# Kernel optimization log

Measured on AMD Instinct MI355X. Metric: run time of the kernel, lower is better.

## Reference

```python
import jax, jax.numpy as jnp
import numpy as np

D, A, V, H, FFH = 512, 256, 256, 1, 256
B, S, VOCAB = 4096, 50, 100000


def _layer_norm(x, g, b, eps=1e-6):
    mu = jnp.mean(x, axis=-1, keepdims=True)
    var = jnp.mean((x - mu) ** 2, axis=-1, keepdims=True)
    return (x - mu) / jnp.sqrt(var + eps) * g + b


def setup_inputs() -> dict:
    key = jax.random.key(0)
    ks = jax.random.split(key, 12)
    s = 0.02
    return {
        "embed_table": jax.random.normal(ks[0], (VOCAB, D), jnp.float32),
        "idx": jax.random.randint(ks[1], (B, S), 0, VOCAB, dtype=jnp.int32),
        "lengths": jax.random.randint(ks[2], (B,), 0, S, dtype=jnp.int32),
        "W1": jax.random.normal(ks[3], (D, FFH), jnp.float32) * s,
        "b1": jnp.zeros((FFH,), jnp.float32),
        "W2": jax.random.normal(ks[4], (FFH, D), jnp.float32) * s,
        "b2": jnp.zeros((D,), jnp.float32),
        "ln1_g": jnp.ones((D,), jnp.float32),
        "ln1_b": jnp.zeros((D,), jnp.float32),
        "W_qkv": jax.random.normal(ks[5], (D, 2 * A + V), jnp.float32) * s,
        "b_qkv": jnp.zeros((2 * A + V,), jnp.float32),
        "W_o": jax.random.normal(ks[6], (V, D), jnp.float32) * s,
        "b_o": jnp.zeros((D,), jnp.float32),
        "ln2_g": jnp.ones((D,), jnp.float32),
        "ln2_b": jnp.zeros((D,), jnp.float32),
    }


def reference(embed_table, idx, lengths, W1, b1, W2, b2, ln1_g, ln1_b,
              W_qkv, b_qkv, W_o, b_o, ln2_g, ln2_b):
    # neighbor validity mask; guaranteed >= 1 valid neighbor per node
    mask = jnp.arange(S)[None, :] <= lengths[:, None]          # [B,S] bool

    # irregular gather of neighbor embeddings into padded tensor
    x = embed_table[idx]                                       # [B,S,D]

    # FeedForward (relu -> linear) + residual + LayerNorm
    ff = jnp.maximum(jnp.einsum('bsd,df->bsf', x, W1) + b1, 0.0)
    ff = jnp.einsum('bsf,fd->bsd', ff, W2) + b2
    ff = _layer_norm(ff + x, ln1_g, ln1_b)                     # [B,S,D]

    # MultiHeadSelfAttention (combined QKV projection)
    qkv = jnp.einsum('bsd,dc->bsc', ff, W_qkv) + b_qkv         # [B,S,2A+V]
    q, k, v = qkv[..., :A], qkv[..., A:2 * A], qkv[..., 2 * A:]
    q = q.reshape(B, S, H, A // H)
    k = k.reshape(B, S, H, A // H)
    v = v.reshape(B, S, H, V // H)
    scale = jnp.asarray(np.sqrt(D // H), q.dtype)              # AllenNLP scale
    scores = jnp.einsum('bqhd,bkhd->bhqk', q / scale, k)       # [B,H,S,S]
    scores = jnp.where(mask[:, None, None, :], scores, jnp.asarray(-1e9, scores.dtype))
    attn = jax.nn.softmax(scores, axis=-1)
    ctx = jnp.einsum('bhqk,bkhd->bqhd', attn, v).reshape(B, S, V)
    attn_out = jnp.einsum('bsv,vd->bsd', ctx, W_o) + b_o

    out = _layer_norm(attn_out + ff, ln2_g, ln2_b)             # [B,S,D]

    # masked mean pool over neighbors
    m = mask[..., None].astype(out.dtype)                      # [B,S,1]
    pooled = jnp.sum(out * m, axis=1) / jnp.maximum(jnp.sum(m, axis=1), 1e-13)
    return pooled                                              # [B,D]
```

## Files before the change

### kernel.cpp

```cpp
#include <hip/hip_runtime.h>

typedef __bf16 bf16x8 __attribute__((ext_vector_type(8)));
typedef float float4v __attribute__((ext_vector_type(4)));
typedef unsigned short ushort4v __attribute__((ext_vector_type(4)));
typedef unsigned short ushort8v __attribute__((ext_vector_type(8)));

#define K_D 512
#define K_S 50

__device__ __forceinline__ float b2f(unsigned short u) {
  union { unsigned int u32; float f; } v; v.u32 = ((unsigned int)u) << 16; return v.f;
}
__device__ __forceinline__ unsigned short f2b(float f) {
  __bf16 h = (__bf16)f;
  return __builtin_bit_cast(unsigned short, h);
}

__device__ __forceinline__ bf16x8 ldfrag(const unsigned short* buf, int E, int r0, int k0, int lane) {
  int row = r0 + (lane & 15);
  int kb = (k0 + ((lane >> 4) << 3)) << 1;
  return *(const bf16x8*)(buf + row * E + ((kb ^ ((row & 7) << 4)) >> 1));
}

__global__ void prep_weights(const float* __restrict__ src, unsigned short* __restrict__ dst,
                             int K, int N) {
  int KT = K >> 5;
  int total = (N >> 4) * KT * 64;
  int t = blockIdx.x * blockDim.x + threadIdx.x;
  if (t >= total) return;
  int l = t & 63;
  int kt = (t >> 6) % KT;
  int nt = (t >> 6) / KT;
  int kbase = kt * 32 + ((l >> 4) << 3);
  int col = nt * 16 + (l & 15);
  ushort8v o;
  #pragma unroll
  for (int j = 0; j < 8; ++j) o[j] = f2b(src[(size_t)(kbase + j) * N + col]);
  *(ushort8v*)(dst + (size_t)t * 8) = o;
}

template<int NT, int KS, int MT, int SLOTS, int APRE>
__device__ __forceinline__ void mmN(const unsigned short* Ab, int EA,
                                    const bf16x8* __restrict__ Wf, int wnb, int KT, int l,
                                    float4v* acc) {
  if constexpr (SLOTS == 2) {
    bf16x8 p0[NT], p1[NT];
    #pragma unroll
    for (int n = 0; n < NT; ++n) {
      p0[n] = Wf[(size_t)((wnb + n) * KT) * 64 + l];
      p1[n] = Wf[(size_t)((wnb + n) * KT + 1) * 64 + l];
    }
    bf16x8 a0[MT], a1[MT];
    if constexpr (APRE) {
      #pragma unroll
      for (int m = 0; m < MT; ++m) {
        a0[m] = ldfrag(Ab, EA, m * 16, 0, l);
        a1[m] = ldfrag(Ab, EA, m * 16, 32, l);
      }
    }
    #pragma unroll 1
    for (int kt = 0; kt < KS; kt += 2) {
      {
        if constexpr (!APRE) {
          #pragma unroll
          for (int m = 0; m < MT; ++m) a0[m] = ldfrag(Ab, EA, m * 16, kt * 32, l);
        }
        #pragma unroll
        for (int n = 0; n < NT; ++n) {
          #pragma unroll
          for (int m = 0; m < MT; ++m)
            acc[m * NT + n] = __builtin_amdgcn_mfma_f32_16x16x32_bf16(a0[m], p0[n], acc[m * NT + n], 0, 0, 0);
        }
        if (kt + 2 < KS) {
          #pragma unroll
          for (int n = 0; n < NT; ++n)
            p0[n] = Wf[(size_t)((wnb + n) * KT + kt + 2) * 64 + l];
          if constexpr (APRE) {
            #pragma unroll
            for (int m = 0; m < MT; ++m) a0[m] = ldfrag(Ab, EA, m * 16, (kt + 2) * 32, l);
          }
        }
      }
      {
        if constexpr (!APRE) {
          #pragma unroll
          for (int m = 0; m < MT; ++m) a1[m] = ldfrag(Ab, EA, m * 16, (kt + 1) * 32, l);
        }
        #pragma unroll
        for (int n = 0; n < NT; ++n) {
          #pragma unroll
          for (int m = 0; m < MT; ++m)
            acc[m * NT + n] = __builtin_amdgcn_mfma_f32_16x16x32_bf16(a1[m], p1[n], acc[m * NT + n], 0, 0, 0);
        }
        if (kt + 3 < KS) {
          #pragma unroll
          for (int n = 0; n < NT; ++n)
            p1[n] = Wf[(size_t)((wnb + n) * KT + kt + 3) * 64 + l];
          if constexpr (APRE) {
            #pragma unroll
            for (int m = 0; m < MT; ++m) a1[m] = ldfrag(Ab, EA, m * 16, (kt + 3) * 32, l);
          }
        }
      }
    }
  } else {
    bf16x8 bn[NT];
    #pragma unroll
    for (int n = 0; n < NT; ++n) bn[n] = Wf[(size_t)((wnb + n) * KT) * 64 + l];
    #pragma unroll 1
    for (int kt = 0; kt < KS; ++kt) {
      bf16x8 a[MT];
      #pragma unroll
      for (int m = 0; m < MT; ++m) a[m] = ldfrag(Ab, EA, m * 16, kt * 32, l);
      #pragma unroll
      for (int n = 0; n < NT; ++n) {
        #pragma unroll
        for (int m = 0; m < MT; ++m)
          acc[m * NT + n] = __builtin_amdgcn_mfma_f32_16x16x32_bf16(a[m], bn[n], acc[m * NT + n], 0, 0, 0);
      }
      if (kt + 1 < KS) {
        #pragma unroll
        for (int n = 0; n < NT; ++n)
          bn[n] = Wf[(size_t)((wnb + n) * KT + kt + 1) * 64 + l];
      }
    }
  }
}

__device__ __forceinline__ void ln_pass(unsigned short* sXbuf, const float* __restrict__ g,
                                        const float* __restrict__ bb, int w, int l, int nrows) {
  float gv[8], bv[8];
  {
    const float4* g4 = (const float4*)(g + l * 8);
    const float4* b4 = (const float4*)(bb + l * 8);
    float4 a0 = g4[0], a1 = g4[1], c0 = b4[0], c1 = b4[1];
    gv[0] = a0.x; gv[1] = a0.y; gv[2] = a0.z; gv[3] = a0.w;
    gv[4] = a1.x; gv[5] = a1.y; gv[6] = a1.z; gv[7] = a1.w;
    bv[0] = c0.x; bv[1] = c0.y; bv[2] = c0.z; bv[3] = c0.w;
    bv[4] = c1.x; bv[5] = c1.y; bv[6] = c1.z; bv[7] = c1.w;
  }
  #pragma unroll 1
  for (int r = w; r < nrows; r += 16) {
    int e = r * 512 + (((l << 4) ^ ((r & 7) << 4)) >> 1);
    ushort8v x = *(const ushort8v*)(sXbuf + e);
    float v[8];
    float s = 0.f, s2 = 0.f;
    #pragma unroll
    for (int j = 0; j < 8; ++j) { v[j] = b2f(x[j]); s += v[j]; s2 += v[j] * v[j]; }
    #pragma unroll
    for (int off = 1; off < 64; off <<= 1) { s += __shfl_xor(s, off); s2 += __shfl_xor(s2, off); }
    float mu = s * (1.f / 512.f);
    float var = s2 * (1.f / 512.f) - mu * mu;
    float rstd = rsqrtf(var + 1e-6f);
    ushort8v o;
    #pragma unroll
    for (int j = 0; j < 8; ++j) o[j] = f2b((v[j] - mu) * rstd * gv[j] + bv[j]);
    *(ushort8v*)(sXbuf + e) = o;
  }
}

template<int MT>
__device__ __forceinline__ void body(
    unsigned short* sX, unsigned short* sQ, unsigned short* sK,
    float* sS, unsigned short* sP,
    const float* __restrict__ embed, const int* __restrict__ gidx,
    const float* __restrict__ b1, const float* __restrict__ b2,
    const float* __restrict__ ln1g, const float* __restrict__ ln1b,
    const float* __restrict__ bqkv, const float* __restrict__ bo,
    const float* __restrict__ ln2g, const float* __restrict__ ln2b,
    const unsigned short* __restrict__ w1f, const unsigned short* __restrict__ w2f,
    const unsigned short* __restrict__ wqkvf, const unsigned short* __restrict__ wof,
    float* __restrict__ out, int tid, int w, int l, int b, int len) {

  constexpr int S2 = (MT <= 3) ? 2 : 1;
  constexpr int AP1 = (MT <= 3) ? 1 : 0;
  constexpr int AP2 = (MT <= 2) ? 1 : 0;

  {
    const int sub = tid >> 7;
    const int c0 = (tid & 127) << 2;
    #pragma unroll 2
    for (int it = 0; it < 2 * MT; ++it) {
      int r = it * 8 + sub;
      float4 v = make_float4(0.f, 0.f, 0.f, 0.f);
      if (r <= len) {
        int row = gidx[b * K_S + r];
        v = *(const float4*)(embed + (size_t)row * K_D + c0);
      }
      ushort4v o;
      o[0] = f2b(v.x); o[1] = f2b(v.y); o[2] = f2b(v.z); o[3] = f2b(v.w);
      *(ushort4v*)(sX + r * 512 + (((c0 << 1) ^ ((r & 7) << 4)) >> 1)) = o;
    }
  }
  __syncthreads();

  {
    float4v acc[MT];
    #pragma unroll
    for (int i = 0; i < MT; ++i) acc[i] = (float4v){0.f, 0.f, 0.f, 0.f};
    mmN<1, 16, MT, 2, AP1>(sX, 512, (const bf16x8*)w1f, w, 16, l, acc);
    int col = w * 16 + (l & 15);
    float bias = b1[col];
    #pragma unroll
    for (int m = 0; m < MT; ++m) {
      int r0 = m * 16 + ((l >> 4) << 2);
      #pragma unroll
      for (int j = 0; j < 4; ++j) {
        int r = r0 + j;
        float v = fmaxf(acc[m][j] + bias, 0.f);
        sQ[r * 256 + (((col << 1) ^ ((r & 7) << 4)) >> 1)] = f2b(v);
      }
    }
  }
  __syncthreads();

  {
    float4v acc[2 * MT];
    #pragma unroll
    for (int i = 0; i < 2 * MT; ++i) acc[i] = (float4v){0.f, 0.f, 0.f, 0.f};
    mmN<2, 8, MT, S2, AP2>(sQ, 256, (const bf16x8*)w2f, w * 2, 8, l, acc);
    #pragma unroll
    for (int n = 0; n < 2; ++n) {
      int col = (w * 2 + n) * 16 + (l & 15);
      float bias = b2[col];
      #pragma unroll
      for (int m = 0; m < MT; ++m) {
        int r0 = m * 16 + ((l >> 4) << 2);
        #pragma unroll
        for (int j = 0; j < 4; ++j) {
          int r = r0 + j;
          int e = r * 512 + (((col << 1) ^ ((r & 7) << 4)) >> 1);
          float v = acc[m * 2 + n][j] + bias + b2f(sX[e]);
          sX[e] = f2b(v);
        }
      }
    }
  }
  __syncthreads();
  ln_pass(sX, ln1g, ln1b, w, l, 16 * MT);
  __syncthreads();

  {
    const bf16x8* Wf = (const bf16x8*)wqkvf;
    float4v accQ[MT], accK[MT];
    #pragma unroll
    for (int i = 0; i < MT; ++i) {
      accQ[i] = (float4v){0.f, 0.f, 0.f, 0.f};
      accK[i] = (float4v){0.f, 0.f, 0.f, 0.f};
    }
    const size_t baseQ = (size_t)(w) * 16 * 64 + l;
    const size_t baseK = (size_t)(16 + w) * 16 * 64 + l;
    if constexpr (MT <= 2) {
      bf16x8 q0 = Wf[baseQ],       k0 = Wf[baseK];
      bf16x8 q1 = Wf[baseQ + 64],  k1 = Wf[baseK + 64];
      bf16x8 a0[MT], a1[MT];
      #pragma unroll
      for (int m = 0; m < MT; ++m) {
        a0[m] = ldfrag(sX, 512, m * 16, 0, l);
        a1[m] = ldfrag(sX, 512, m * 16, 32, l);
      }
      #pragma unroll 1
      for (int kt = 0; kt < 16; kt += 2) {
        {
          #pragma unroll
          for (int m = 0; m < MT; ++m) accQ[m] = __builtin_amdgcn_mfma_f32_16x16x32_bf16(a0[m], q0, accQ[m], 0, 0, 0);
          #pragma unroll
          for (int m = 0; m < MT; ++m) accK[m] = __builtin_amdgcn_mfma_f32_16x16x32_bf16(a0[m], k0, accK[m], 0, 0, 0);
          if (kt + 2 < 16) {
            q0 = Wf[baseQ + (size_t)(kt + 2) * 64];
            k0 = Wf[baseK + (size_t)(kt + 2) * 64];
            #pragma unroll
            for (int m = 0; m < MT; ++m) a0[m] = ldfrag(sX, 512, m * 16, (kt + 2) * 32, l);
          }
        }
        {
          #pragma unroll
          for (int m = 0; m < MT; ++m) accQ[m] = __builtin_amdgcn_mfma_f32_16x16x32_bf16(a1[m], q1, accQ[m], 0, 0, 0);
          #pragma unroll
          for (int m = 0; m < MT; ++m) accK[m] = __builtin_amdgcn_mfma_f32_16x16x32_bf16(a1[m], k1, accK[m], 0, 0, 0);
          if (kt + 3 < 16) {
            q1 = Wf[baseQ + (size_t)(kt + 3) * 64];
            k1 = Wf[baseK + (size_t)(kt + 3) * 64];
            #pragma unroll
            for (int m = 0; m < MT; ++m) a1[m] = ldfrag(sX, 512, m * 16, (kt + 3) * 32, l);
          }
        }
      }
    } else {
      bf16x8 q0 = Wf[baseQ], k0 = Wf[baseK];
      #pragma unroll 1
      for (int kt = 0; kt < 16; ++kt) {
        bf16x8 a[MT];
        #pragma unroll
        for (int m = 0; m < MT; ++m) a[m] = ldfrag(sX, 512, m * 16, kt * 32, l);
        #pragma unroll
        for (int m = 0; m < MT; ++m) accQ[m] = __builtin_amdgcn_mfma_f32_16x16x32_bf16(a[m], q0, accQ[m], 0, 0, 0);
        #pragma unroll
        for (int m = 0; m < MT; ++m) accK[m] = __builtin_amdgcn_mfma_f32_16x16x32_bf16(a[m], k0, accK[m], 0, 0, 0);
        if (kt + 1 < 16) {
          q0 = Wf[baseQ + (size_t)(kt + 1) * 64];
          k0 = Wf[baseK + (size_t)(kt + 1) * 64];
        }
      }
    }
    const float qscale = 0.044194173824159216f;
    int col = w * 16 + (l & 15);
    float biasQ = bqkv[col];
    float biasK = bqkv[256 + col];
    #pragma unroll
    for (int m = 0; m < MT; ++m) {
      int r0 = m * 16 + ((l >> 4) << 2);
      #pragma unroll
      for (int j = 0; j < 4; ++j) {
        int r = r0 + j;
        sQ[r * 256 + (((col << 1) ^ ((r & 7) << 4)) >> 1)] = f2b((accQ[m][j] + biasQ) * qscale);
        sK[r * 256 + (((col << 1) ^ ((r & 7) << 4)) >> 1)] = f2b(accK[m][j] + biasK);
      }
    }
  }
  __syncthreads();

  if ((w >> 2) < MT) {
    float4v acc = (float4v){0.f, 0.f, 0.f, 0.f};
    int n0 = (w & 3) * 16;
    int m0 = (w >> 2) * 16;
    bf16x8 b0 = ldfrag(sK, 256, n0, 0, l),  aq0 = ldfrag(sQ, 256, m0, 0, l);
    bf16x8 b1 = ldfrag(sK, 256, n0, 32, l), aq1 = ldfrag(sQ, 256, m0, 32, l);
    #pragma unroll 1
    for (int kt = 0; kt < 8; kt += 2) {
      acc = __builtin_amdgcn_mfma_f32_16x16x32_bf16(aq0, b0, acc, 0, 0, 0);
      if (kt + 2 < 8) {
        b0 = ldfrag(sK, 256, n0, (kt + 2) * 32, l);
        aq0 = ldfrag(sQ, 256, m0, (kt + 2) * 32, l);
      }
      acc = __builtin_amdgcn_mfma_f32_16x16x32_bf16(aq1, b1, acc, 0, 0, 0);
      if (kt + 3 < 8) {
        b1 = ldfrag(sK, 256, n0, (kt + 3) * 32, l);
        aq1 = ldfrag(sQ, 256, m0, (kt + 3) * 32, l);
      }
    }
    int col = n0 + (l & 15);
    int r0 = m0 + ((l >> 4) << 2);
    #pragma unroll
    for (int j = 0; j < 4; ++j) {
      int r = r0 + j;
      sS[r * 64 + (((col << 2) ^ ((r & 7) << 4)) >> 2)] = acc[j];
    }
  }
  float4v accV[MT];
  {
    #pragma unroll
    for (int i = 0; i < MT; ++i) accV[i] = (float4v){0.f, 0.f, 0.f, 0.f};
    mmN<1, 16, MT, 2, AP1>(sX, 512, (const bf16x8*)wqkvf, 32 + w, 16, l, accV);
  }
  __syncthreads();

  {
    const bool valid = (l <= len);
    #pragma unroll 1
    for (int r = w; r < 16 * MT; r += 16) {
      float s = valid ? sS[r * 64 + (((l << 2) ^ ((r & 7) << 4)) >> 2)] : -1e30f;
      float mx = s;
      #pragma unroll
      for (int off = 1; off < 64; off <<= 1) mx = fmaxf(mx, __shfl_xor(mx, off));
      float p = valid ? __expf(s - mx) : 0.f;
      float sum = p;
      #pragma unroll
      for (int off = 1; off < 64; off <<= 1) sum += __shfl_xor(sum, off);
      sP[r * 64 + (((l << 1) ^ ((r & 7) << 4)) >> 1)] = f2b(p / sum);
    }
    int c = w * 16 + (l & 15);
    float biasV = bqkv[512 + c];
    #pragma unroll
    for (int m = 0; m < MT; ++m) {
      int r0 = m * 16 + ((l >> 4) << 2);
      ushort4v o;
      #pragma unroll
      for (int j = 0; j < 4; ++j) o[j] = f2b(accV[m][j] + biasV);
      *(ushort4v*)(sK + c * 64 + (((r0 << 1) ^ ((c & 7) << 4)) >> 1)) = o;
    }
    #pragma unroll
    for (int m = MT; m < 4; ++m) {
      int r0 = m * 16 + ((l >> 4) << 2);
      ushort4v o; o[0] = 0; o[1] = 0; o[2] = 0; o[3] = 0;
      *(ushort4v*)(sK + c * 64 + (((r0 << 1) ^ ((c & 7) << 4)) >> 1)) = o;
    }
  }
  __syncthreads();

  {
    float4v acc[MT];
    #pragma unroll
    for (int i = 0; i < MT; ++i) acc[i] = (float4v){0.f, 0.f, 0.f, 0.f};
    #pragma unroll
    for (int kt = 0; kt < 2; ++kt) {
      bf16x8 bfr = ldfrag(sK, 64, w * 16, kt * 32, l);
      #pragma unroll
      for (int m = 0; m < MT; ++m) {
        bf16x8 a = ldfrag(sP, 64, m * 16, kt * 32, l);
        acc[m] = __builtin_amdgcn_mfma_f32_16x16x32_bf16(a, bfr, acc[m], 0, 0, 0);
      }
    }
    int col = w * 16 + (l & 15);
    #pragma unroll
    for (int m = 0; m < MT; ++m) {
      int r0 = m * 16 + ((l >> 4) << 2);
      #pragma unroll
      for (int j = 0; j < 4; ++j) {
        int r = r0 + j;
        sQ[r * 256 + (((col << 1) ^ ((r & 7) << 4)) >> 1)] = f2b(acc[m][j]);
      }
    }
  }
  __syncthreads();

  {
    float4v acc[2 * MT];
    #pragma unroll
    for (int i = 0; i < 2 * MT; ++i) acc[i] = (float4v){0.f, 0.f, 0.f, 0.f};
    mmN<2, 8, MT, S2, AP2>(sQ, 256, (const bf16x8*)wof, w * 2, 8, l, acc);
    #pragma unroll
    for (int n = 0; n < 2; ++n) {
      int col = (w * 2 + n) * 16 + (l & 15);
      float bias = bo[col];
      #pragma unroll
      for (int m = 0; m < MT; ++m) {
        int r0 = m * 16 + ((l >> 4) << 2);
        #pragma unroll
        for (int j = 0; j < 4; ++j) {
          int r = r0 + j;
          int e = r * 512 + (((col << 1) ^ ((r & 7) << 4)) >> 1);
          float v = acc[m * 2 + n][j] + bias + b2f(sX[e]);
          sX[e] = f2b(v);
        }
      }
    }
  }
  __syncthreads();
  ln_pass(sX, ln2g, ln2b, w, l, 16 * MT);
  __syncthreads();

  {
    int col = tid & 511;
    int half = tid >> 9;
    float sum = 0.f;
    for (int s = half; s <= len; s += 2)
      sum += b2f(sX[s * 512 + (((col << 1) ^ ((s & 7) << 4)) >> 1)]);
    if (half) sS[col] = sum;
    __syncthreads();
    if (!half) out[(size_t)b * K_D + col] = (sum + sS[col]) / (float)(len + 1);
  }
}

__global__ __launch_bounds__(1024, 4)
void fused_block(
    const float* __restrict__ embed, const int* __restrict__ gidx,
    const int* __restrict__ lengths,
    const float* __restrict__ b1, const float* __restrict__ b2,
    const float* __restrict__ ln1g, const float* __restrict__ ln1b,
    const float* __restrict__ bqkv, const float* __restrict__ bo,
    const float* __restrict__ ln2g, const float* __restrict__ ln2b,
    const unsigned short* __restrict__ w1f, const unsigned short* __restrict__ w2f,
    const unsigned short* __restrict__ wqkvf, const unsigned short* __restrict__ wof,
    float* __restrict__ out) {
  __shared__ unsigned short sX[64 * 512];
  __shared__ unsigned short sQ[64 * 256];
  __shared__ unsigned short sK[64 * 256];
  __shared__ float sS[64 * 64];
  __shared__ unsigned short sP[64 * 64];

  const int tid = (int)threadIdx.x;
  const int w = tid >> 6;
  const int l = tid & 63;
  const int b = (int)blockIdx.x;
  const int len = lengths[b];
  const int mt = (len + 16) >> 4;

  switch (mt) {
    case 1: body<1>(sX, sQ, sK, sS, sP, embed, gidx, b1, b2, ln1g, ln1b, bqkv, bo,
                    ln2g, ln2b, w1f, w2f, wqkvf, wof, out, tid, w, l, b, len); break;
    case 2: body<2>(sX, sQ, sK, sS, sP, embed, gidx, b1, b2, ln1g, ln1b, bqkv, bo,
                    ln2g, ln2b, w1f, w2f, wqkvf, wof, out, tid, w, l, b, len); break;
    case 3: body<3>(sX, sQ, sK, sS, sP, embed, gidx, b1, b2, ln1g, ln1b, bqkv, bo,
                    ln2g, ln2b, w1f, w2f, wqkvf, wof, out, tid, w, l, b, len); break;
    default: body<4>(sX, sQ, sK, sS, sP, embed, gidx, b1, b2, ln1g, ln1b, bqkv, bo,
                     ln2g, ln2b, w1f, w2f, wqkvf, wof, out, tid, w, l, b, len); break;
  }
}

extern "C" void kernel_launch(void* const* d_in, const int* in_sizes, int n_in,
                              void* d_out, int out_size, void* d_ws, size_t ws_size,
                              hipStream_t stream) {
  (void)in_sizes; (void)n_in; (void)out_size; (void)ws_size;
  const float* embed = (const float*)d_in[0];
  const int* idx = (const int*)d_in[1];
  const int* lengths = (const int*)d_in[2];
  const float* W1 = (const float*)d_in[3];
  const float* b1 = (const float*)d_in[4];
  const float* W2 = (const float*)d_in[5];
  const float* b2 = (const float*)d_in[6];
  const float* ln1g = (const float*)d_in[7];
  const float* ln1b = (const float*)d_in[8];
  const float* Wqkv = (const float*)d_in[9];
  const float* bqkv = (const float*)d_in[10];
  const float* Wo = (const float*)d_in[11];
  const float* bo = (const float*)d_in[12];
  const float* ln2g = (const float*)d_in[13];
  const float* ln2b = (const float*)d_in[14];

  unsigned short* ws = (unsigned short*)d_ws;
  unsigned short* w1f = ws;
  unsigned short* w2f = ws + 131072;
  unsigned short* wqkvf = ws + 262144;
  unsigned short* wof = ws + 655360;

  prep_weights<<<64, 256, 0, stream>>>(W1, w1f, 512, 256);
  prep_weights<<<64, 256, 0, stream>>>(W2, w2f, 256, 512);
  prep_weights<<<192, 256, 0, stream>>>(Wqkv, wqkvf, 512, 768);
  prep_weights<<<64, 256, 0, stream>>>(Wo, wof, 256, 512);

  fused_block<<<4096, 1024, 0, stream>>>(embed, idx, lengths, b1, b2, ln1g, ln1b,
                                         bqkv, bo, ln2g, ln2b, w1f, w2f, wqkvf, wof,
                                         (float*)d_out);
}
```

Baseline: 512.0 us.

## Split fused kernel into per-tile-count launches with right-sized shared memory

Replaces the single fused kernel, which dispatched on tile count but always reserved maximum shared memory, with four templated kernels launched back to back. Each sizes its LDS buffers to its own row count and exits early for batches of other lengths. The short-sequence cases also shrink the padded V/score tile to 32 keys. This aims to raise blocks per CU for short neighbor lists, at the cost of four full-grid launches whose blocks mostly exit immediately.

```diff
diff --git a/kernel.cpp b/kernel.cpp
--- a/kernel.cpp
+++ b/kernel.cpp
@@ -20,6 +20,12 @@
   int row = r0 + (lane & 15);
   int kb = (k0 + ((lane >> 4) << 3)) << 1;
   return *(const bf16x8*)(buf + row * E + ((kb ^ ((row & 7) << 4)) >> 1));
+}
+__device__ __forceinline__ bf16x8 ldfragm(const unsigned short* buf, int E, int r0, int k0,
+                                          int lane, int mask) {
+  int row = r0 + (lane & 15);
+  int kb = (k0 + ((lane >> 4) << 3)) << 1;
+  return *(const bf16x8*)(buf + row * E + ((kb ^ ((row & mask) << 4)) >> 1));
 }
 
 __global__ void prep_weights(const float* __restrict__ src, unsigned short* __restrict__ dst,
@@ -160,17 +166,33 @@
 }
 
 template<int MT>
-__device__ __forceinline__ void body(
-    unsigned short* sX, unsigned short* sQ, unsigned short* sK,
-    float* sS, unsigned short* sP,
+__global__ __launch_bounds__(1024, 4) void fused_mt(
     const float* __restrict__ embed, const int* __restrict__ gidx,
+    const int* __restrict__ lengths,
     const float* __restrict__ b1, const float* __restrict__ b2,
     const float* __restrict__ ln1g, const float* __restrict__ ln1b,
     const float* __restrict__ bqkv, const float* __restrict__ bo,
     const float* __restrict__ ln2g, const float* __restrict__ ln2b,
     const unsigned short* __restrict__ w1f, const unsigned short* __restrict__ w2f,
     const unsigned short* __restrict__ wqkvf, const unsigned short* __restrict__ wof,
-    float* __restrict__ out, int tid, int w, int l, int b, int len) {
+    float* __restrict__ out) {
+  constexpr int ROWS = 16 * MT;
+  constexpr int KVP = (MT <= 2) ? 32 : 64;
+  constexpr int SWM = (MT <= 2) ? 3 : 7;
+  constexpr int SKE = (ROWS * 256 > 256 * KVP) ? ROWS * 256 : 256 * KVP;
+
+  __shared__ unsigned short sX[ROWS * 512];
+  __shared__ unsigned short sQ[ROWS * 256];
+  __shared__ unsigned short sK[SKE];
+  __shared__ float sS[ROWS * 64];
+  __shared__ unsigned short sP[ROWS * 64];
+
+  const int tid = (int)threadIdx.x;
+  const int w = tid >> 6;
+  const int l = tid & 63;
+  const int b = (int)blockIdx.x;
+  const int len = lengths[b];
+  if (((len + 16) >> 4) != MT) return;
 
   constexpr int S2 = (MT <= 3) ? 2 : 1;
   constexpr int AP1 = (MT <= 3) ? 1 : 0;
@@ -237,7 +259,7 @@
     }
   }
   __syncthreads();
-  ln_pass(sX, ln1g, ln1b, w, l, 16 * MT);
+  ln_pass(sX, ln1g, ln1b, w, l, ROWS);
   __syncthreads();
 
   {
@@ -320,31 +342,42 @@
   }
   __syncthreads();
 
-  if ((w >> 2) < MT) {
-    float4v acc = (float4v){0.f, 0.f, 0.f, 0.f};
-    int n0 = (w & 3) * 16;
-    int m0 = (w >> 2) * 16;
-    bf16x8 b0 = ldfrag(sK, 256, n0, 0, l),  aq0 = ldfrag(sQ, 256, m0, 0, l);
-    bf16x8 b1 = ldfrag(sK, 256, n0, 32, l), aq1 = ldfrag(sQ, 256, m0, 32, l);
-    #pragma unroll 1
-    for (int kt = 0; kt < 8; kt += 2) {
-      acc = __builtin_amdgcn_mfma_f32_16x16x32_bf16(aq0, b0, acc, 0, 0, 0);
-      if (kt + 2 < 8) {
-        b0 = ldfrag(sK, 256, n0, (kt + 2) * 32, l);
-        aq0 = ldfrag(sQ, 256, m0, (kt + 2) * 32, l);
-      }
-      acc = __builtin_amdgcn_mfma_f32_16x16x32_bf16(aq1, b1, acc, 0, 0, 0);
-      if (kt + 3 < 8) {
-        b1 = ldfrag(sK, 256, n0, (kt + 3) * 32, l);
-        aq1 = ldfrag(sQ, 256, m0, (kt + 3) * 32, l);
-      }
-    }
-    int col = n0 + (l & 15);
-    int r0 = m0 + ((l >> 4) << 2);
-    #pragma unroll
-    for (int j = 0; j < 4; ++j) {
-      int r = r0 + j;
-      sS[r * 64 + (((col << 2) ^ ((r & 7) << 4)) >> 2)] = acc[j];
+  {
+    bool doScore;
+    int m0, n0;
+    if constexpr (MT <= 2) {
+      doScore = (w < MT * MT);
+      m0 = (MT == 1) ? 0 : (w >> 1) * 16;
+      n0 = (MT == 1) ? 0 : (w & 1) * 16;
+    } else {
+      doScore = ((w >> 2) < MT);
+      m0 = (w >> 2) * 16;
+      n0 = (w & 3) * 16;
+    }
+    if (doScore) {
+      float4v acc = (float4v){0.f, 0.f, 0.f, 0.f};
+      bf16x8 b0 = ldfrag(sK, 256, n0, 0, l),  aq0 = ldfrag(sQ, 256, m0, 0, l);
+      bf16x8 b1 = ldfrag(sK, 256, n0, 32, l), aq1 = ldfrag(sQ, 256, m0, 32, l);
+      #pragma unroll 1
+      for (int kt = 0; kt < 8; kt += 2) {
+        acc = __builtin_amdgcn_mfma_f32_16x16x32_bf16(aq0, b0, acc, 0, 0, 0);
+        if (kt + 2 < 8) {
+          b0 = ldfrag(sK, 256, n0, (kt + 2) * 32, l);
+          aq0 = ldfrag(sQ, 256, m0, (kt + 2) * 32, l);
+        }
+        acc = __builtin_amdgcn_mfma_f32_16x16x32_bf16(aq1, b1, acc, 0, 0, 0);
+        if (kt + 3 < 8) {
+          b1 = ldfrag(sK, 256, n0, (kt + 3) * 32, l);
+          aq1 = ldfrag(sQ, 256, m0, (kt + 3) * 32, l);
+        }
+      }
+      int col = n0 + (l & 15);
+      int r0 = m0 + ((l >> 4) << 2);
+      #pragma unroll
+      for (int j = 0; j < 4; ++j) {
+        int r = r0 + j;
+        sS[r * 64 + (((col << 2) ^ ((r & 7) << 4)) >> 2)] = acc[j];
+      }
     }
   }
   float4v accV[MT];
@@ -358,7 +391,7 @@
   {
     const bool valid = (l <= len);
     #pragma unroll 1
-    for (int r = w; r < 16 * MT; r += 16) {
+    for (int r = w; r < ROWS; r += 16) {
       float s = valid ? sS[r * 64 + (((l << 2) ^ ((r & 7) << 4)) >> 2)] : -1e30f;
       float mx = s;
       #pragma unroll
@@ -377,13 +410,13 @@
       ushort4v o;
       #pragma unroll
       for (int j = 0; j < 4; ++j) o[j] = f2b(accV[m][j] + biasV);
-      *(ushort4v*)(sK + c * 64 + (((r0 << 1) ^ ((c & 7) << 4)) >> 1)) = o;
-    }
-    #pragma unroll
-    for (int m = MT; m < 4; ++m) {
+      *(ushort4v*)(sK + c * KVP + (((r0 << 1) ^ ((c & SWM) << 4)) >> 1)) = o;
+    }
+    #pragma unroll
+    for (int m = MT; m < KVP / 16; ++m) {
       int r0 = m * 16 + ((l >> 4) << 2);
       ushort4v o; o[0] = 0; o[1] = 0; o[2] = 0; o[3] = 0;
-      *(ushort4v*)(sK + c * 64 + (((r0 << 1) ^ ((c & 7) << 4)) >> 1)) = o;
+      *(ushort4v*)(sK + c * KVP + (((r0 << 1) ^ ((c & SWM) << 4)) >> 1)) = o;
     }
   }
   __syncthreads();
@@ -393,8 +426,8 @@
     #pragma unroll
     for (int i = 0; i < MT; ++i) acc[i] = (float4v){0.f, 0.f, 0.f, 0.f};
     #pragma unroll
-    for (int kt = 0; kt < 2; ++kt) {
-      bf16x8 bfr = ldfrag(sK, 64, w * 16, kt * 32, l);
+    for (int kt = 0; kt < KVP / 32; ++kt) {
+      bf16x8 bfr = ldfragm(sK, KVP, w * 16, kt * 32, l, SWM);
       #pragma unroll
       for (int m = 0; m < MT; ++m) {
         bf16x8 a = ldfrag(sP, 64, m * 16, kt * 32, l);
@@ -437,7 +470,7 @@
     }
   }
   __syncthreads();
-  ln_pass(sX, ln2g, ln2b, w, l, 16 * MT);
+  ln_pass(sX, ln2g, ln2b, w, l, ROWS);
   __syncthreads();
 
   {
@@ -449,42 +482,6 @@
     if (half) sS[col] = sum;
     __syncthreads();
     if (!half) out[(size_t)b * K_D + col] = (sum + sS[col]) / (float)(len + 1);
-  }
-}
-
-__global__ __launch_bounds__(1024, 4)
-void fused_block(
-    const float* __restrict__ embed, const int* __restrict__ gidx,
-    const int* __restrict__ lengths,
-    const float* __restrict__ b1, const float* __restrict__ b2,
-    const float* __restrict__ ln1g, const float* __restrict__ ln1b,
-    const float* __restrict__ bqkv, const float* __restrict__ bo,
-    const float* __restrict__ ln2g, const float* __restrict__ ln2b,
-    const unsigned short* __restrict__ w1f, const unsigned short* __restrict__ w2f,
-    const unsigned short* __restrict__ wqkvf, const unsigned short* __restrict__ wof,
-    float* __restrict__ out) {
-  __shared__ unsigned short sX[64 * 512];
-  __shared__ unsigned short sQ[64 * 256];
-  __shared__ unsigned short sK[64 * 256];
-  __shared__ float sS[64 * 64];
-  __shared__ unsigned short sP[64 * 64];
-
-  const int tid = (int)threadIdx.x;
-  const int w = tid >> 6;
-  const int l = tid & 63;
-  const int b = (int)blockIdx.x;
-  const int len = lengths[b];
-  const int mt = (len + 16) >> 4;
-
-  switch (mt) {
-    case 1: body<1>(sX, sQ, sK, sS, sP, embed, gidx, b1, b2, ln1g, ln1b, bqkv, bo,
-                    ln2g, ln2b, w1f, w2f, wqkvf, wof, out, tid, w, l, b, len); break;
-    case 2: body<2>(sX, sQ, sK, sS, sP, embed, gidx, b1, b2, ln1g, ln1b, bqkv, bo,
-                    ln2g, ln2b, w1f, w2f, wqkvf, wof, out, tid, w, l, b, len); break;
-    case 3: body<3>(sX, sQ, sK, sS, sP, embed, gidx, b1, b2, ln1g, ln1b, bqkv, bo,
-                    ln2g, ln2b, w1f, w2f, wqkvf, wof, out, tid, w, l, b, len); break;
-    default: body<4>(sX, sQ, sK, sS, sP, embed, gidx, b1, b2, ln1g, ln1b, bqkv, bo,
-                     ln2g, ln2b, w1f, w2f, wqkvf, wof, out, tid, w, l, b, len); break;
   }
 }
 
@@ -519,7 +516,16 @@
   prep_weights<<<192, 256, 0, stream>>>(Wqkv, wqkvf, 512, 768);
   prep_weights<<<64, 256, 0, stream>>>(Wo, wof, 256, 512);
 
-  fused_block<<<4096, 1024, 0, stream>>>(embed, idx, lengths, b1, b2, ln1g, ln1b,
+  fused_mt<1><<<4096, 1024, 0, stream>>>(embed, idx, lengths, b1, b2, ln1g, ln1b,
                                          bqkv, bo, ln2g, ln2b, w1f, w2f, wqkvf, wof,
                                          (float*)d_out);
-}
+  fused_mt<2><<<4096, 1024, 0, stream>>>(embed, idx, lengths, b1, b2, ln1g, ln1b,
+                                         bqkv, bo, ln2g, ln2b, w1f, w2f, wqkvf, wof,
+                                         (float*)d_out);
+  fused_mt<3><<<4096, 1024, 0, stream>>>(embed, idx, lengths, b1, b2, ln1g, ln1b,
+                                         bqkv, bo, ln2g, ln2b, w1f, w2f, wqkvf, wof,
+                                         (float*)d_out);
+  fused_mt<4><<<4096, 1024, 0, stream>>>(embed, idx, lengths, b1, b2, ln1g, ln1b,
+                                         bqkv, bo, ln2g, ln2b, w1f, w2f, wqkvf, wof,
+                                         (float*)d_out);
+}
```

After: 753.8 us. +47.2%, slower.

## Fuse V projection into QK loop and split-K score computation for small tiles

Applied to the files above, without the earlier changes.

For small tile counts (MT<=2), the V projection is computed in the same k-loop as Q and K, so each A fragment loaded from shared memory is reused across three MFMAs. The QK^T score product is split over k across all 16 waves, with partial sums written to scratch shared memory and reduced during softmax, so waves are no longer left idle when there are few row tiles. The V-transpose buffer uses a narrower 32-column padding with a matching swizzle mask for short sequences. In exchange the code is longer, adds a barrier and a partial-sum reduction, and holds more registers during the fused loop.

```diff
diff --git a/kernel.cpp b/kernel.cpp
--- a/kernel.cpp
+++ b/kernel.cpp
@@ -20,6 +20,12 @@
   int row = r0 + (lane & 15);
   int kb = (k0 + ((lane >> 4) << 3)) << 1;
   return *(const bf16x8*)(buf + row * E + ((kb ^ ((row & 7) << 4)) >> 1));
+}
+__device__ __forceinline__ bf16x8 ldfragm(const unsigned short* buf, int E, int r0, int k0,
+                                          int lane, int mask) {
+  int row = r0 + (lane & 15);
+  int kb = (k0 + ((lane >> 4) << 3)) << 1;
+  return *(const bf16x8*)(buf + row * E + ((kb ^ ((row & mask) << 4)) >> 1));
 }
 
 __global__ void prep_weights(const float* __restrict__ src, unsigned short* __restrict__ dst,
@@ -172,6 +178,9 @@
     const unsigned short* __restrict__ wqkvf, const unsigned short* __restrict__ wof,
     float* __restrict__ out, int tid, int w, int l, int b, int len) {
 
+  constexpr int ROWS = 16 * MT;
+  constexpr int KVP = (MT <= 2) ? 32 : 64;
+  constexpr int SWM = (MT <= 2) ? 3 : 7;
   constexpr int S2 = (MT <= 3) ? 2 : 1;
   constexpr int AP1 = (MT <= 3) ? 1 : 0;
   constexpr int AP2 = (MT <= 2) ? 1 : 0;
@@ -237,10 +246,14 @@
     }
   }
   __syncthreads();
-  ln_pass(sX, ln1g, ln1b, w, l, 16 * MT);
+  ln_pass(sX, ln1g, ln1b, w, l, ROWS);
   __syncthreads();
 
-  {
+  float4v accV[MT];
+  #pragma unroll
+  for (int i = 0; i < MT; ++i) accV[i] = (float4v){0.f, 0.f, 0.f, 0.f};
+
+  if constexpr (MT <= 2) {
     const bf16x8* Wf = (const bf16x8*)wqkvf;
     float4v accQ[MT], accK[MT];
     #pragma unroll
@@ -248,45 +261,142 @@
       accQ[i] = (float4v){0.f, 0.f, 0.f, 0.f};
       accK[i] = (float4v){0.f, 0.f, 0.f, 0.f};
     }
-    const size_t baseQ = (size_t)(w) * 16 * 64 + l;
-    const size_t baseK = (size_t)(16 + w) * 16 * 64 + l;
-    if constexpr (MT <= 2) {
-      bf16x8 q0 = Wf[baseQ],       k0 = Wf[baseK];
-      bf16x8 q1 = Wf[baseQ + 64],  k1 = Wf[baseK + 64];
-      bf16x8 a0[MT], a1[MT];
+    const size_t bQ = (size_t)(w) * 16 * 64 + l;
+    const size_t bK = (size_t)(16 + w) * 16 * 64 + l;
+    const size_t bV = (size_t)(32 + w) * 16 * 64 + l;
+    bf16x8 q0 = Wf[bQ],      k0 = Wf[bK],      v0 = Wf[bV];
+    bf16x8 q1 = Wf[bQ + 64], k1 = Wf[bK + 64], v1 = Wf[bV + 64];
+    #pragma unroll 1
+    for (int kt = 0; kt < 16; kt += 2) {
+      {
+        bf16x8 a[MT];
+        #pragma unroll
+        for (int m = 0; m < MT; ++m) a[m] = ldfrag(sX, 512, m * 16, kt * 32, l);
+        #pragma unroll
+        for (int m = 0; m < MT; ++m) accQ[m] = __builtin_amdgcn_mfma_f32_16x16x32_bf16(a[m], q0, accQ[m], 0, 0, 0);
+        #pragma unroll
+        for (int m = 0; m < MT; ++m) accK[m] = __builtin_amdgcn_mfma_f32_16x16x32_bf16(a[m], k0, accK[m], 0, 0, 0);
+        #pragma unroll
+        for (int m = 0; m < MT; ++m) accV[m] = __builtin_amdgcn_mfma_f32_16x16x32_bf16(a[m], v0, accV[m], 0, 0, 0);
+        if (kt + 2 < 16) {
+          q0 = Wf[bQ + (size_t)(kt + 2) * 64];
+          k0 = Wf[bK + (size_t)(kt + 2) * 64];
+          v0 = Wf[bV + (size_t)(kt + 2) * 64];
+        }
+      }
+      {
+        bf16x8 a[MT];
+        #pragma unroll
+        for (int m = 0; m < MT; ++m) a[m] = ldfrag(sX, 512, m * 16, (kt + 1) * 32, l);
+        #pragma unroll
+        for (int m = 0; m < MT; ++m) accQ[m] = __builtin_amdgcn_mfma_f32_16x16x32_bf16(a[m], q1, accQ[m], 0, 0, 0);
+        #pragma unroll
+        for (int m = 0; m < MT; ++m) accK[m] = __builtin_amdgcn_mfma_f32_16x16x32_bf16(a[m], k1, accK[m], 0, 0, 0);
+        #pragma unroll
+        for (int m = 0; m < MT; ++m) accV[m] = __builtin_amdgcn_mfma_f32_16x16x32_bf16(a[m], v1, accV[m], 0, 0, 0);
+        if (kt + 3 < 16) {
+          q1 = Wf[bQ + (size_t)(kt + 3) * 64];
+          k1 = Wf[bK + (size_t)(kt + 3) * 64];
+          v1 = Wf[bV + (size_t)(kt + 3) * 64];
+        }
+      }
+    }
+    const float qscale = 0.044194173824159216f;
+    int col = w * 16 + (l & 15);
+    float biasQ = bqkv[col];
+    float biasK = bqkv[256 + col];
+    #pragma unroll
+    for (int m = 0; m < MT; ++m) {
+      int r0 = m * 16 + ((l >> 4) << 2);
+      #pragma unroll
+      for (int j = 0; j < 4; ++j) {
+        int r = r0 + j;
+        sQ[r * 256 + (((col << 1) ^ ((r & 7) << 4)) >> 1)] = f2b((accQ[m][j] + biasQ) * qscale);
+        sK[r * 256 + (((col << 1) ^ ((r & 7) << 4)) >> 1)] = f2b(accK[m][j] + biasK);
+      }
+    }
+    __syncthreads();
+
+    {
+      float* sS4 = (float*)(sX + 32 * 512);
+      constexpr int NP = (MT == 1) ? 8 : 4;
+      constexpr int KTP = 8 / NP;
+      bool doS = (MT == 1) ? (w < 8) : true;
+      if (doS) {
+        int tile = (MT == 1) ? 0 : (w >> 2);
+        int p = (MT == 1) ? w : (w & 3);
+        int m0 = (MT == 1) ? 0 : (tile >> 1) * 16;
+        int n0 = (MT == 1) ? 0 : (tile & 1) * 16;
+        float4v acc = (float4v){0.f, 0.f, 0.f, 0.f};
+        #pragma unroll
+        for (int kk = 0; kk < KTP; ++kk) {
+          int kt = p * KTP + kk;
+          bf16x8 bfr = ldfrag(sK, 256, n0, kt * 32, l);
+          bf16x8 a = ldfrag(sQ, 256, m0, kt * 32, l);
+          acc = __builtin_amdgcn_mfma_f32_16x16x32_bf16(a, bfr, acc, 0, 0, 0);
+        }
+        int col2 = n0 + (l & 15);
+        int r0 = m0 + ((l >> 4) << 2);
+        #pragma unroll
+        for (int j = 0; j < 4; ++j) {
+          int r = r0 + j;
+          sS4[(p * ROWS + r) * 64 + (((col2 << 2) ^ ((r & 7) << 4)) >> 2)] = acc[j];
+        }
+      }
+    }
+    __syncthreads();
+
+    {
+      const float* sS4 = (const float*)(sX + 32 * 512);
+      constexpr int NP = (MT == 1) ? 8 : 4;
+      const bool valid = (l <= len);
+      #pragma unroll 1
+      for (int r = w; r < ROWS; r += 16) {
+        float s = -1e30f;
+        if (valid) {
+          int e = (((l << 2) ^ ((r & 7) << 4)) >> 2);
+          s = 0.f;
+          #pragma unroll
+          for (int p = 0; p < NP; ++p) s += sS4[(p * ROWS + r) * 64 + e];
+        }
+        float mx = s;
+        #pragma unroll
+        for (int off = 1; off < 64; off <<= 1) mx = fmaxf(mx, __shfl_xor(mx, off));
+        float p = valid ? __expf(s - mx) : 0.f;
+        float sum = p;
+        #pragma unroll
+        for (int off = 1; off < 64; off <<= 1) sum += __shfl_xor(sum, off);
+        sP[r * 64 + (((l << 1) ^ ((r & 7) << 4)) >> 1)] = f2b(p / sum);
+      }
+      int c = w * 16 + (l & 15);
+      float biasV = bqkv[512 + c];
       #pragma unroll
       for (int m = 0; m < MT; ++m) {
-        a0[m] = ldfrag(sX, 512, m * 16, 0, l);
-        a1[m] = ldfrag(sX, 512, m * 16, 32, l);
-      }
-      #pragma unroll 1
-      for (int kt = 0; kt < 16; kt += 2) {
-        {
-          #pragma unroll
-          for (int m = 0; m < MT; ++m) accQ[m] = __builtin_amdgcn_mfma_f32_16x16x32_bf16(a0[m], q0, accQ[m], 0, 0, 0);
-          #pragma unroll
-          for (int m = 0; m < MT; ++m) accK[m] = __builtin_amdgcn_mfma_f32_16x16x32_bf16(a0[m], k0, accK[m], 0, 0, 0);
-          if (kt + 2 < 16) {
-            q0 = Wf[baseQ + (size_t)(kt + 2) * 64];
-            k0 = Wf[baseK + (size_t)(kt + 2) * 64];
-            #pragma unroll
-            for (int m = 0; m < MT; ++m) a0[m] = ldfrag(sX, 512, m * 16, (kt + 2) * 32, l);
-          }
-        }
-        {
-          #pragma unroll
-          for (int m = 0; m < MT; ++m) accQ[m] = __builtin_amdgcn_mfma_f32_16x16x32_bf16(a1[m], q1, accQ[m], 0, 0, 0);
-          #pragma unroll
-          for (int m = 0; m < MT; ++m) accK[m] = __builtin_amdgcn_mfma_f32_16x16x32_bf16(a1[m], k1, accK[m], 0, 0, 0);
-          if (kt + 3 < 16) {
-            q1 = Wf[baseQ + (size_t)(kt + 3) * 64];
-            k1 = Wf[baseK + (size_t)(kt + 3) * 64];
-            #pragma unroll
-            for (int m = 0; m < MT; ++m) a1[m] = ldfrag(sX, 512, m * 16, (kt + 3) * 32, l);
-          }
-        }
-      }
-    } else {
+        int r0 = m * 16 + ((l >> 4) << 2);
+        ushort4v o;
+        #pragma unroll
+        for (int j = 0; j < 4; ++j) o[j] = f2b(accV[m][j] + biasV);
+        *(ushort4v*)(sK + c * KVP + (((r0 << 1) ^ ((c & SWM) << 4)) >> 1)) = o;
+      }
+      #pragma unroll
+      for (int m = MT; m < KVP / 16; ++m) {
+        int r0 = m * 16 + ((l >> 4) << 2);
+        ushort4v o; o[0] = 0; o[1] = 0; o[2] = 0; o[3] = 0;
+        *(ushort4v*)(sK + c * KVP + (((r0 << 1) ^ ((c & SWM) << 4)) >> 1)) = o;
+      }
+    }
+    __syncthreads();
+  } else {
+    {
+      const bf16x8* Wf = (const bf16x8*)wqkvf;
+      float4v accQ[MT], accK[MT];
+      #pragma unroll
+      for (int i = 0; i < MT; ++i) {
+        accQ[i] = (float4v){0.f, 0.f, 0.f, 0.f};
+        accK[i] = (float4v){0.f, 0.f, 0.f, 0.f};
+      }
+      const size_t baseQ = (size_t)(w) * 16 * 64 + l;
+      const size_t baseK = (size_t)(16 + w) * 16 * 64 + l;
       bf16x8 q0 = Wf[baseQ], k0 = Wf[baseK];
       #pragma unroll 1
       for (int kt = 0; kt < 16; ++kt) {
@@ -302,99 +412,96 @@
           k0 = Wf[baseK + (size_t)(kt + 1) * 64];
         }
       }
-    }
-    const float qscale = 0.044194173824159216f;
-    int col = w * 16 + (l & 15);
-    float biasQ = bqkv[col];
-    float biasK = bqkv[256 + col];
-    #pragma unroll
-    for (int m = 0; m < MT; ++m) {
-      int r0 = m * 16 + ((l >> 4) << 2);
+      const float qscale = 0.044194173824159216f;
+      int col = w * 16 + (l & 15);
+      float biasQ = bqkv[col];
+      float biasK = bqkv[256 + col];
+      #pragma unroll
+      for (int m = 0; m < MT; ++m) {
+        int r0 = m * 16 + ((l >> 4) << 2);
+        #pragma unroll
+        for (int j = 0; j < 4; ++j) {
+          int r = r0 + j;
+          sQ[r * 256 + (((col << 1) ^ ((r & 7) << 4)) >> 1)] = f2b((accQ[m][j] + biasQ) * qscale);
+          sK[r * 256 + (((col << 1) ^ ((r & 7) << 4)) >> 1)] = f2b(accK[m][j] + biasK);
+        }
+      }
+    }
+    __syncthreads();
+
+    if ((w >> 2) < MT) {
+      float4v acc = (float4v){0.f, 0.f, 0.f, 0.f};
+      int n0 = (w & 3) * 16;
+      int m0 = (w >> 2) * 16;
+      bf16x8 b0 = ldfrag(sK, 256, n0, 0, l),  aq0 = ldfrag(sQ, 256, m0, 0, l);
+      bf16x8 b1 = ldfrag(sK, 256, n0, 32, l), aq1 = ldfrag(sQ, 256, m0, 32, l);
+      #pragma unroll 1
+      for (int kt = 0; kt < 8; kt += 2) {
+        acc = __builtin_amdgcn_mfma_f32_16x16x32_bf16(aq0, b0, acc, 0, 0, 0);
+        if (kt + 2 < 8) {
+          b0 = ldfrag(sK, 256, n0, (kt + 2) * 32, l);
+          aq0 = ldfrag(sQ, 256, m0, (kt + 2) * 32, l);
+        }
+        acc = __builtin_amdgcn_mfma_f32_16x16x32_bf16(aq1, b1, acc, 0, 0, 0);
+        if (kt + 3 < 8) {
+          b1 = ldfrag(sK, 256, n0, (kt + 3) * 32, l);
+          aq1 = ldfrag(sQ, 256, m0, (kt + 3) * 32, l);
+        }
+      }
+      int col = n0 + (l & 15);
+      int r0 = m0 + ((l >> 4) << 2);
       #pragma unroll
       for (int j = 0; j < 4; ++j) {
         int r = r0 + j;
-        sQ[r * 256 + (((col << 1) ^ ((r & 7) << 4)) >> 1)] = f2b((accQ[m][j] + biasQ) * qscale);
-        sK[r * 256 + (((col << 1) ^ ((r & 7) << 4)) >> 1)] = f2b(accK[m][j] + biasK);
-      }
-    }
-  }
-  __syncthreads();
-
-  if ((w >> 2) < MT) {
-    float4v acc = (float4v){0.f, 0.f, 0.f, 0.f};
-    int n0 = (w & 3) * 16;
-    int m0 = (w >> 2) * 16;
-    bf16x8 b0 = ldfrag(sK, 256, n0, 0, l),  aq0 = ldfrag(sQ, 256, m0, 0, l);
-    bf16x8 b1 = ldfrag(sK, 256, n0, 32, l), aq1 = ldfrag(sQ, 256, m0, 32, l);
-    #pragma unroll 1
-    for (int kt = 0; kt < 8; kt += 2) {
-      acc = __builtin_amdgcn_mfma_f32_16x16x32_bf16(aq0, b0, acc, 0, 0, 0);
-      if (kt + 2 < 8) {
-        b0 = ldfrag(sK, 256, n0, (kt + 2) * 32, l);
-        aq0 = ldfrag(sQ, 256, m0, (kt + 2) * 32, l);
-      }
-      acc = __builtin_amdgcn_mfma_f32_16x16x32_bf16(aq1, b1, acc, 0, 0, 0);
-      if (kt + 3 < 8) {
-        b1 = ldfrag(sK, 256, n0, (kt + 3) * 32, l);
-        aq1 = ldfrag(sQ, 256, m0, (kt + 3) * 32, l);
-      }
-    }
-    int col = n0 + (l & 15);
-    int r0 = m0 + ((l >> 4) << 2);
-    #pragma unroll
-    for (int j = 0; j < 4; ++j) {
-      int r = r0 + j;
-      sS[r * 64 + (((col << 2) ^ ((r & 7) << 4)) >> 2)] = acc[j];
-    }
-  }
-  float4v accV[MT];
-  {
-    #pragma unroll
-    for (int i = 0; i < MT; ++i) accV[i] = (float4v){0.f, 0.f, 0.f, 0.f};
-    mmN<1, 16, MT, 2, AP1>(sX, 512, (const bf16x8*)wqkvf, 32 + w, 16, l, accV);
-  }
-  __syncthreads();
-
-  {
-    const bool valid = (l <= len);
-    #pragma unroll 1
-    for (int r = w; r < 16 * MT; r += 16) {
-      float s = valid ? sS[r * 64 + (((l << 2) ^ ((r & 7) << 4)) >> 2)] : -1e30f;
-      float mx = s;
-      #pragma unroll
-      for (int off = 1; off < 64; off <<= 1) mx = fmaxf(mx, __shfl_xor(mx, off));
-      float p = valid ? __expf(s - mx) : 0.f;
-      float sum = p;
-      #pragma unroll
-      for (int off = 1; off < 64; off <<= 1) sum += __shfl_xor(sum, off);
-      sP[r * 64 + (((l << 1) ^ ((r & 7) << 4)) >> 1)] = f2b(p / sum);
-    }
-    int c = w * 16 + (l & 15);
-    float biasV = bqkv[512 + c];
-    #pragma unroll
-    for (int m = 0; m < MT; ++m) {
-      int r0 = m * 16 + ((l >> 4) << 2);
-      ushort4v o;
-      #pragma unroll
-      for (int j = 0; j < 4; ++j) o[j] = f2b(accV[m][j] + biasV);
-      *(ushort4v*)(sK + c * 64 + (((r0 << 1) ^ ((c & 7) << 4)) >> 1)) = o;
-    }
-    #pragma unroll
-    for (int m = MT; m < 4; ++m) {
-      int r0 = m * 16 + ((l >> 4) << 2);
-      ushort4v o; o[0] = 0; o[1] = 0; o[2] = 0; o[3] = 0;
-      *(ushort4v*)(sK + c * 64 + (((r0 << 1) ^ ((c & 7) << 4)) >> 1)) = o;
-    }
-  }
-  __syncthreads();
+        sS[r * 64 + (((col << 2) ^ ((r & 7) << 4)) >> 2)] = acc[j];
+      }
+    }
+    {
+      mmN<1, 16, MT, 2, AP1>(sX, 512, (const bf16x8*)wqkvf, 32 + w, 16, l, accV);
+    }
+    __syncthreads();
+
+    {
+      const bool valid = (l <= len);
+      #pragma unroll 1
+      for (int r = w; r < ROWS; r += 16) {
+        float s = valid ? sS[r * 64 + (((l << 2) ^ ((r & 7) << 4)) >> 2)] : -1e30f;
+        float mx = s;
+        #pragma unroll
+        for (int off = 1; off < 64; off <<= 1) mx = fmaxf(mx, __shfl_xor(mx, off));
+        float p = valid ? __expf(s - mx) : 0.f;
+        float sum = p;
+        #pragma unroll
+        for (int off = 1; off < 64; off <<= 1) sum += __shfl_xor(sum, off);
+        sP[r * 64 + (((l << 1) ^ ((r & 7) << 4)) >> 1)] = f2b(p / sum);
+      }
+      int c = w * 16 + (l & 15);
+      float biasV = bqkv[512 + c];
+      #pragma unroll
+      for (int m = 0; m < MT; ++m) {
+        int r0 = m * 16 + ((l >> 4) << 2);
+        ushort4v o;
+        #pragma unroll
+        for (int j = 0; j < 4; ++j) o[j] = f2b(accV[m][j] + biasV);
+        *(ushort4v*)(sK + c * KVP + (((r0 << 1) ^ ((c & SWM) << 4)) >> 1)) = o;
+      }
+      #pragma unroll
+      for (int m = MT; m < KVP / 16; ++m) {
+        int r0 = m * 16 + ((l >> 4) << 2);
+        ushort4v o; o[0] = 0; o[1] = 0; o[2] = 0; o[3] = 0;
+        *(ushort4v*)(sK + c * KVP + (((r0 << 1) ^ ((c & SWM) << 4)) >> 1)) = o;
+      }
+    }
+    __syncthreads();
+  }
 
   {
     float4v acc[MT];
     #pragma unroll
     for (int i = 0; i < MT; ++i) acc[i] = (float4v){0.f, 0.f, 0.f, 0.f};
     #pragma unroll
-    for (int kt = 0; kt < 2; ++kt) {
-      bf16x8 bfr = ldfrag(sK, 64, w * 16, kt * 32, l);
+    for (int kt = 0; kt < KVP / 32; ++kt) {
+      bf16x8 bfr = ldfragm(sK, KVP, w * 16, kt * 32, l, SWM);
       #pragma unroll
       for (int m = 0; m < MT; ++m) {
         bf16x8 a = ldfrag(sP, 64, m * 16, kt * 32, l);
@@ -437,7 +544,7 @@
     }
   }
   __syncthreads();
-  ln_pass(sX, ln2g, ln2b, w, l, 16 * MT);
+  ln_pass(sX, ln2g, ln2b, w, l, ROWS);
   __syncthreads();
 
   {
```

Result: slower. 528.9 us (+3.3%).
